# Optimization experiments

Hardware: AMD Instinct MI355X
Metric: run time of the kernel (lower is better)

Reference implementation:

```python
import jax, jax.numpy as jnp
import numpy as np

H, NB, D = 16, 64, 1024
HID = 64  # gate MLP hidden width


def setup_inputs() -> dict:
    key = jax.random.key(0)
    ks = jax.random.split(key, 10)
    B, T = 4, 2048
    delta = jax.random.normal(ks[0], (B, T, H, NB), dtype=jnp.float32)
    content_emb = jax.random.normal(ks[1], (B, T, D), dtype=jnp.float32)
    omega = jax.random.normal(ks[2], (H, NB), dtype=jnp.float32)
    # learned parameters
    log_Q = jnp.zeros((H, NB), dtype=jnp.float32)
    log_R = jnp.zeros((H, NB), dtype=jnp.float32)
    log_sigma0 = jnp.full((H, NB), -2.0, dtype=jnp.float32)
    W1 = jax.random.normal(ks[3], (D, HID), dtype=jnp.float32) / np.sqrt(D)
    b1 = jnp.zeros((HID,), dtype=jnp.float32)
    W2 = jax.random.normal(ks[4], (HID, H * NB), dtype=jnp.float32) / np.sqrt(HID)
    b2 = jnp.zeros((H * NB,), dtype=jnp.float32)
    return {"delta": delta, "content_emb": content_emb, "omega": omega,
            "log_Q": log_Q, "log_R": log_R, "log_sigma0": log_sigma0,
            "W1": W1, "b1": b1, "W2": W2, "b2": b2}


def reference(delta, content_emb, omega, log_Q, log_R, log_sigma0, W1, b1, W2, b2):
    B, T, _, _ = delta.shape
    Q = jnp.exp(log_Q)            # (H, NB)
    R = jnp.exp(log_R)            # (H, NB)
    sigma0 = jnp.exp(log_sigma0)  # (H, NB)

    theta_sq = (delta * omega) ** 2  # (B, T, H, NB)

    # landmark gate MLP (exact GELU, as torch default)
    h = jax.nn.gelu(content_emb @ W1 + b1, approximate=False)  # (B, T, HID)
    gates = jax.nn.sigmoid(h @ W2 + b2).reshape(B, T, H, NB)

    def step(sigma, xs):
        theta_sq_t, gate_t = xs  # (B, H, NB) each
        sigma = sigma + Q * theta_sq_t
        K = sigma / (sigma + R)
        sigma = sigma * (1.0 - gate_t * K)
        return sigma, sigma

    init = jnp.broadcast_to(sigma0, (B, H, NB))
    xs = (jnp.swapaxes(theta_sq, 0, 1), jnp.swapaxes(gates, 0, 1))  # (T, B, H, NB)
    _, sigma_seq = jax.lax.scan(step, init, xs)
    sigma = jnp.swapaxes(sigma_seq, 0, 1)  # (B, T, H, NB)
    return sigma, gates
```

## Files before the change

kernel.cpp:

```cpp
#include <hip/hip_runtime.h>
#include <math.h>

#define H_   16
#define NB_  64
#define D_   1024
#define HID_ 64
#define B_   4
#define T_   2048
#define ROWS (B_*T_)
#define HNB  (H_*NB_)

typedef short v8s __attribute__((ext_vector_type(8)));
typedef float v4f __attribute__((ext_vector_type(4)));

__device__ __forceinline__ float gelu_exact(float x) {
    return 0.5f * x * (1.0f + erff(x * 0.7071067811865476f));
}
__device__ __forceinline__ float sigmoidf(float x) {
    return 1.0f / (1.0f + expf(-x));
}
__device__ __forceinline__ ushort f2bf(float x) {
    union { float f; unsigned u; } v; v.f = x;
    unsigned r = v.u + 0x7fffu + ((v.u >> 16) & 1u);
    return (ushort)(r >> 16);
}

__global__ __launch_bounds__(256) void k_prep(const float* __restrict__ W1,
                                              const float* __restrict__ W2,
                                              ushort* __restrict__ w1t,
                                              ushort* __restrict__ w2t) {
    __shared__ float ls[64][65];
    const int t   = threadIdx.x;
    const int blk = blockIdx.x;
    if (blk < 16) {
        const int k0 = blk * 64;
        #pragma unroll
        for (int q = 0; q < 4; ++q) {
            int idx = q * 256 + t;
            int r = idx >> 4, c4 = idx & 15;
            *(float4*)&ls[r][c4 * 4] =
                *(const float4*)&W1[(size_t)(k0 + r) * 64 + c4 * 4];
        }
        __syncthreads();
        const int col = t >> 2, kq = t & 3;
        ushort out[16];
        #pragma unroll
        for (int e = 0; e < 16; ++e) out[e] = f2bf(ls[kq * 16 + e][col]);
        *(uint4*)&w1t[(size_t)col * 1024 + k0 + kq * 16]     = *(uint4*)&out[0];
        *(uint4*)&w1t[(size_t)col * 1024 + k0 + kq * 16 + 8] = *(uint4*)&out[8];
    } else {
        const int n0 = (blk - 16) * 64;
        #pragma unroll
        for (int q = 0; q < 4; ++q) {
            int idx = q * 256 + t;
            int r = idx >> 4, c4 = idx & 15;
            *(float4*)&ls[r][c4 * 4] =
                *(const float4*)&W2[(size_t)r * HNB + n0 + c4 * 4];
        }
        __syncthreads();
        const int n = t >> 2, kq = t & 3;
        ushort out[16];
        #pragma unroll
        for (int e = 0; e < 16; ++e) out[e] = f2bf(ls[kq * 16 + e][n]);
        *(uint4*)&w2t[(size_t)(n0 + n) * 64 + kq * 16]     = *(uint4*)&out[0];
        *(uint4*)&w2t[(size_t)(n0 + n) * 64 + kq * 16 + 8] = *(uint4*)&out[8];
    }
}

__global__ __launch_bounds__(256) void k_gemm1_mfma(const float* __restrict__ X,
                                                    const ushort* __restrict__ w1t,
                                                    const float* __restrict__ b1,
                                                    ushort* __restrict__ hbuf) {
    __shared__ ushort Al[16 * 128];
    __shared__ ushort Bl[64 * 128];
    const int t    = threadIdx.x;
    const int r0   = blockIdx.x * 16;
    const int w    = t >> 6;
    const int lane = t & 63;
    const int lo   = lane & 15;
    const int hi   = lane >> 4;
    const int arow = t >> 4, aseg = t & 15;
    const int brow = t >> 2, bseg = t & 3;

    v4f acc = {0.f,0.f,0.f,0.f};

    for (int c = 0; c < 8; ++c) {
        float xv[8];
        const float* xp = &X[(size_t)(r0 + arow) * D_ + c * 128 + aseg * 8];
        *(float4*)&xv[0] = *(const float4*)&xp[0];
        *(float4*)&xv[4] = *(const float4*)&xp[4];
        ushort wv[32];
        const ushort* wp = &w1t[(size_t)brow * 1024 + c * 128 + bseg * 32];
        #pragma unroll
        for (int i = 0; i < 4; ++i) *(uint4*)&wv[i*8] = *(const uint4*)&wp[i*8];

        __syncthreads();
        {
            const int k = aseg * 8;
            union { ushort u[8]; v8s v; } pa;
            #pragma unroll
            for (int e = 0; e < 8; ++e) pa.u[e] = f2bf(xv[e]);
            *(v8s*)&Al[arow * 128 + (k ^ ((arow & 7) << 3))] = pa.v;
        }
        #pragma unroll
        for (int j8 = 0; j8 < 4; ++j8) {
            const int k = bseg * 32 + j8 * 8;
            *(v8s*)&Bl[brow * 128 + (k ^ ((brow & 7) << 3))] = *(v8s*)&wv[j8 * 8];
        }
        __syncthreads();

        #pragma unroll
        for (int kk = 0; kk < 4; ++kk) {
            const int k  = kk * 32 + hi * 8;
            const int sw = k ^ ((lo & 7) << 3);
            v8s af = *(v8s*)&Al[lo * 128 + sw];
            v8s bf = *(v8s*)&Bl[(w * 16 + lo) * 128 + sw];
            acc = __builtin_amdgcn_mfma_f32_16x16x32_bf16(af, bf, acc, 0, 0, 0);
        }
    }
    const int col = w * 16 + lo;
    const float bb = b1[col];
    #pragma unroll
    for (int j = 0; j < 4; ++j) {
        const int row = r0 + hi * 4 + j;
        hbuf[(size_t)row * HID_ + col] = f2bf(gelu_exact(acc[j] + bb));
    }
}

__global__ __launch_bounds__(256) void k_gemm2_mfma(const ushort* __restrict__ hbuf,
                                                    const ushort* __restrict__ w2t,
                                                    const float* __restrict__ b2,
                                                    float* __restrict__ gates) {
    __shared__ ushort Ah[64 * 64];
    __shared__ ushort Bh[256 * 64];
    const int t    = threadIdx.x;
    const int r0   = (blockIdx.x >> 2) * 64;
    const int n0   = (blockIdx.x & 3) * 256;
    const int w    = t >> 6;
    const int lane = t & 63;
    const int lo   = lane & 15;
    const int hi   = lane >> 4;

    {
        const int row = t >> 2, seg = t & 3;
        uint4 v0 = *(const uint4*)&hbuf[(size_t)(r0 + row) * 64 + seg * 16];
        uint4 v1 = *(const uint4*)&hbuf[(size_t)(r0 + row) * 64 + seg * 16 + 8];
        const int sw = (row & 7) << 3;
        *(uint4*)&Ah[row * 64 + ((seg * 16) ^ sw)]     = v0;
        *(uint4*)&Ah[row * 64 + ((seg * 16 + 8) ^ sw)] = v1;
    }
    #pragma unroll
    for (int q = 0; q < 4; ++q) {
        const int pi  = q * 256 + t;
        const int n   = pi >> 2, seg = pi & 3;
        uint4 v0 = *(const uint4*)&w2t[(size_t)(n0 + n) * 64 + seg * 16];
        uint4 v1 = *(const uint4*)&w2t[(size_t)(n0 + n) * 64 + seg * 16 + 8];
        const int sw = (n & 7) << 3;
        *(uint4*)&Bh[n * 64 + ((seg * 16) ^ sw)]     = v0;
        *(uint4*)&Bh[n * 64 + ((seg * 16 + 8) ^ sw)] = v1;
    }
    __syncthreads();

    v4f acc[4][4];
    #pragma unroll
    for (int mt = 0; mt < 4; ++mt)
        #pragma unroll
        for (int nt = 0; nt < 4; ++nt) acc[mt][nt] = (v4f){0.f,0.f,0.f,0.f};

    #pragma unroll
    for (int kc = 0; kc < 2; ++kc) {
        const int k  = kc * 32 + hi * 8;
        const int sw = k ^ ((lo & 7) << 3);
        v8s af[4];
        #pragma unroll
        for (int mt = 0; mt < 4; ++mt)
            af[mt] = *(v8s*)&Ah[(mt * 16 + lo) * 64 + sw];
        #pragma unroll
        for (int nt = 0; nt < 4; ++nt) {
            v8s bf = *(v8s*)&Bh[(w * 64 + nt * 16 + lo) * 64 + sw];
            #pragma unroll
            for (int mt = 0; mt < 4; ++mt)
                acc[mt][nt] = __builtin_amdgcn_mfma_f32_16x16x32_bf16(af[mt], bf, acc[mt][nt], 0, 0, 0);
        }
    }

    #pragma unroll
    for (int nt = 0; nt < 4; ++nt) {
        const int col = n0 + w * 64 + nt * 16 + lo;
        const float bb = b2[col];
        #pragma unroll
        for (int mt = 0; mt < 4; ++mt) {
            #pragma unroll
            for (int j = 0; j < 4; ++j) {
                const int row = r0 + mt * 16 + hi * 4 + j;
                gates[(size_t)row * HNB + col] = sigmoidf(acc[mt][nt][j] + bb);
            }
        }
    }
}

#define TT_    32
#define SEGK   8
#define SEGLEN (T_/SEGK)
#define WARMT  2

#define PHASE_SYNC() { \
    asm volatile("s_waitcnt lgkmcnt(0)" ::: "memory"); \
    __builtin_amdgcn_s_barrier(); \
    asm volatile("" ::: "memory"); }

#define LD8(A, G, grp) { \
    _Pragma("unroll") \
    for (int u = 0; u < 8; ++u) { \
        A[u] = pa[((grp)*8 + u) * 128]; \
        G[u] = pa[((grp)*8 + u) * 128 + 64]; \
    } }

#define CP8(A, G, grp) { \
    _Pragma("unroll") \
    for (int u = 0; u < 8; ++u) { \
        float a   = A[u]; \
        float omg = G[u]; \
        float aR  = a + R; \
        float pc  = fmaf(omg, a, R); \
        float den = sigma + aR; \
        float s   = sigma + a; \
        float pp  = fmaf(omg, sigma, pc); \
        float rc  = __builtin_amdgcn_rcpf(den); \
        float tt  = s * pp; \
        sigma     = tt * rc; \
        ps[((grp)*8 + u) * 64] = sigma; \
    } }

#define DLOAD(tile) { \
    const int t0_ = tstart + (tile) * TT_; \
    _Pragma("unroll") \
    for (int it = 0; it < 8; ++it) \
        dreg[it] = *(const float4*)&dp[(size_t)(t0_ + it * 4 + rg) * HNB]; }

__global__ __launch_bounds__(256) void k_scan_seg4(
        const float* __restrict__ delta,
        const float* __restrict__ gates,
        const float* __restrict__ omega,
        const float* __restrict__ log_Q,
        const float* __restrict__ log_R,
        const float* __restrict__ log_s0,
        float* __restrict__ sig) {
    __shared__ float tg_lds[2][TT_][2][64];
    __shared__ float sg_lds[2][TT_][64];
    const int tid = threadIdx.x;
    const int blk = blockIdx.x;
    const int bh  = blk >> 3;
    const int seg = blk & 7;
    const int b   = bh >> 4;
    const int h   = bh & 15;
    const size_t base = (size_t)b * T_ * HNB + h * NB_;
    const int wv   = tid >> 6;
    const int lane = tid & 63;

    const int warm   = (seg == 0) ? 0 : WARMT;
    const int ntiles = SEGLEN / TT_ + warm;
    const int tstart = seg * SEGLEN - warm * TT_;

    float R = 0.f, sigma = 0.f;
    float sc0=0,sc1=0,sc2=0,sc3=0;
    const int col4 = lane & 15;
    const int rg   = lane >> 4;
    const float* dp = 0;
    float4 dreg[8];

    if (wv == 0) {
        const int hn = h * NB_ + lane;
        R     = expf(log_R[hn]);
        sigma = expf(log_s0[hn]);
    } else if (wv == 1) {
        const int hn4 = h * NB_ + col4 * 4;
        float4 om4 = *(const float4*)&omega[hn4];
        float4 lq4 = *(const float4*)&log_Q[hn4];
        sc0 = expf(lq4.x) * om4.x * om4.x;
        sc1 = expf(lq4.y) * om4.y * om4.y;
        sc2 = expf(lq4.z) * om4.z * om4.z;
        sc3 = expf(lq4.w) * om4.w * om4.w;
        dp = delta + base + col4 * 4;
        DLOAD(0);
    } else if (wv == 2) {
        dp = gates + base + col4 * 4;
        DLOAD(0);
    }

    for (int p = 0; p <= ntiles + 1; ++p) {
        if (wv == 0) {
            if (p >= 1 && p <= ntiles) {
                const int buf = (p - 1) & 1;
                const float* pa = &tg_lds[buf][0][0][lane];
                float*       ps = &sg_lds[buf][0][lane];
                float a0[8], g0[8], a1[8], g1[8];
                LD8(a0, g0, 0);
                LD8(a1, g1, 1);
                CP8(a0, g0, 0); LD8(a0, g0, 2);
                CP8(a1, g1, 1); LD8(a1, g1, 3);
                CP8(a0, g0, 2);
                CP8(a1, g1, 3);
            }
        } else if (wv == 1) {
            if (p < ntiles) {
                const int buf = p & 1;
                #pragma unroll
                for (int it = 0; it < 8; ++it) {
                    const int row = it * 4 + rg;
                    float4 d = dreg[it];
                    float4 a;
                    a.x = (sc0 * d.x) * d.x;
                    a.y = (sc1 * d.y) * d.y;
                    a.z = (sc2 * d.z) * d.z;
                    a.w = (sc3 * d.w) * d.w;
                    *(float4*)&tg_lds[buf][row][0][col4 * 4] = a;
                }
                if (p + 1 < ntiles) DLOAD(p + 1);
            }
        } else if (wv == 2) {
            if (p < ntiles) {
                const int buf = p & 1;
                #pragma unroll
                for (int it = 0; it < 8; ++it) {
                    const int row = it * 4 + rg;
                    float4 g = dreg[it];
                    float4 o;
                    o.x = 1.0f - g.x; o.y = 1.0f - g.y;
                    o.z = 1.0f - g.z; o.w = 1.0f - g.w;
                    *(float4*)&tg_lds[buf][row][1][col4 * 4] = o;
                }
                if (p + 1 < ntiles) DLOAD(p + 1);
            }
        } else {
            const int tile = p - 2;
            if (tile >= warm && tile < ntiles) {
                const int buf = p & 1;
                const int t0  = tstart + tile * TT_;
                float* op = sig + base + col4 * 4;
                #pragma unroll
                for (int it = 0; it < 8; ++it) {
                    const int row = it * 4 + rg;
                    float4 v = *(const float4*)&sg_lds[buf][row][col4 * 4];
                    *(float4*)&op[(size_t)(t0 + row) * HNB] = v;
                }
            }
        }
        PHASE_SYNC();
    }
}

extern "C" void kernel_launch(void* const* d_in, const int* in_sizes, int n_in,
                              void* d_out, int out_size, void* d_ws, size_t ws_size,
                              hipStream_t stream) {
    const float* delta   = (const float*)d_in[0];
    const float* content = (const float*)d_in[1];
    const float* omega   = (const float*)d_in[2];
    const float* log_Q   = (const float*)d_in[3];
    const float* log_R   = (const float*)d_in[4];
    const float* log_s0  = (const float*)d_in[5];
    const float* W1      = (const float*)d_in[6];
    const float* b1      = (const float*)d_in[7];
    const float* W2      = (const float*)d_in[8];
    const float* b2      = (const float*)d_in[9];

    float* sig_out   = (float*)d_out;
    float* gates_out = sig_out + (size_t)ROWS * HNB;

    const size_t n_h   = (size_t)ROWS * HID_;
    const size_t n_w1t = (size_t)HID_ * D_;
    const size_t n_w2t = (size_t)HNB * HID_;
    const size_t need  = (n_h + n_w1t + n_w2t) * sizeof(ushort);

    ushort *hbuf, *w1t, *w2t;
    if (ws_size >= need) {
        hbuf = (ushort*)d_ws;
    } else {
        hbuf = (ushort*)sig_out;
    }
    w1t = hbuf + n_h;
    w2t = w1t + n_w1t;

    k_prep<<<32, 256, 0, stream>>>(W1, W2, w1t, w2t);
    k_gemm1_mfma<<<ROWS / 16, 256, 0, stream>>>(content, w1t, b1, hbuf);
    k_gemm2_mfma<<<(ROWS / 64) * 4, 256, 0, stream>>>(hbuf, w2t, b2, gates_out);
    k_scan_seg4<<<B_ * H_ * SEGK, 256, 0, stream>>>(delta, gates_out, omega,
                                                    log_Q, log_R, log_s0, sig_out);
}
```

Measured before the change: 55.34 us.

## Feed scan a bf16 copy of gates and remap scan block order

The gate GEMM now also writes a bf16 copy of the sigmoid gates to workspace, and a new scan kernel reads that half-width copy instead of the fp32 gates, unpacking it in a dedicated wave. The block index mapping is also permuted so that consecutive blocks cover different (b,h) pairs. The aim is to cut scan-side memory traffic, at the cost of an extra 16 MB write in the GEMM and reduced gate precision inside the recurrence. The new path only runs when the workspace is large enough; otherwise the old path is used.

```diff
diff --git a/kernel.cpp b/kernel.cpp
--- a/kernel.cpp
+++ b/kernel.cpp
@@ -130,7 +130,8 @@
 __global__ __launch_bounds__(256) void k_gemm2_mfma(const ushort* __restrict__ hbuf,
                                                     const ushort* __restrict__ w2t,
                                                     const float* __restrict__ b2,
-                                                    float* __restrict__ gates) {
+                                                    float* __restrict__ gates,
+                                                    ushort* __restrict__ gbf) {
     __shared__ ushort Ah[64 * 64];
     __shared__ ushort Bh[256 * 64];
     const int t    = threadIdx.x;
@@ -193,7 +194,9 @@
             #pragma unroll
             for (int j = 0; j < 4; ++j) {
                 const int row = r0 + mt * 16 + hi * 4 + j;
-                gates[(size_t)row * HNB + col] = sigmoidf(acc[mt][nt][j] + bb);
+                float gv = sigmoidf(acc[mt][nt][j] + bb);
+                gates[(size_t)row * HNB + col] = gv;
+                if (gbf) gbf[(size_t)row * HNB + col] = f2bf(gv);
             }
         }
     }
@@ -237,6 +240,133 @@
     _Pragma("unroll") \
     for (int it = 0; it < 8; ++it) \
         dreg[it] = *(const float4*)&dp[(size_t)(t0_ + it * 4 + rg) * HNB]; }
+
+#define GLOAD(tile) { \
+    const int t0_ = tstart + (tile) * TT_; \
+    _Pragma("unroll") \
+    for (int it = 0; it < 4; ++it) \
+        greg[it] = *(const uint4*)&gp2[(size_t)(t0_ + it * 8 + rg8) * HNB]; }
+
+__global__ __launch_bounds__(256) void k_scan_seg6(
+        const float* __restrict__ delta,
+        const ushort* __restrict__ gbf,
+        const float* __restrict__ omega,
+        const float* __restrict__ log_Q,
+        const float* __restrict__ log_R,
+        const float* __restrict__ log_s0,
+        float* __restrict__ sig) {
+    __shared__ float tg_lds[2][TT_][2][64];
+    __shared__ float sg_lds[2][TT_][64];
+    const int tid = threadIdx.x;
+    const int blk = blockIdx.x;
+    const int bh  = (blk & 7) * 8 + (blk >> 6);
+    const int seg = (blk >> 3) & 7;
+    const int b   = bh >> 4;
+    const int h   = bh & 15;
+    const size_t base = (size_t)b * T_ * HNB + h * NB_;
+    const int wv   = tid >> 6;
+    const int lane = tid & 63;
+
+    const int warm   = (seg == 0) ? 0 : WARMT;
+    const int ntiles = SEGLEN / TT_ + warm;
+    const int tstart = seg * SEGLEN - warm * TT_;
+
+    float R = 0.f, sigma = 0.f;
+    float sc0=0,sc1=0,sc2=0,sc3=0;
+    const int col4 = lane & 15;
+    const int rg   = lane >> 4;
+    const int col8 = lane & 7;
+    const int rg8  = lane >> 3;
+    const float* dp = 0;
+    const ushort* gp2 = 0;
+    float4 dreg[8];
+    uint4  greg[4];
+
+    if (wv == 0) {
+        const int hn = h * NB_ + lane;
+        R     = expf(log_R[hn]);
+        sigma = expf(log_s0[hn]);
+    } else if (wv == 1) {
+        const int hn4 = h * NB_ + col4 * 4;
+        float4 om4 = *(const float4*)&omega[hn4];
+        float4 lq4 = *(const float4*)&log_Q[hn4];
+        sc0 = expf(lq4.x) * om4.x * om4.x;
+        sc1 = expf(lq4.y) * om4.y * om4.y;
+        sc2 = expf(lq4.z) * om4.z * om4.z;
+        sc3 = expf(lq4.w) * om4.w * om4.w;
+        dp = delta + base + col4 * 4;
+        DLOAD(0);
+    } else if (wv == 2) {
+        gp2 = gbf + base + col8 * 8;
+        GLOAD(0);
+    }
+
+    for (int p = 0; p <= ntiles + 1; ++p) {
+        if (wv == 0) {
+            if (p >= 1 && p <= ntiles) {
+                const int buf = (p - 1) & 1;
+                const float* pa = &tg_lds[buf][0][0][lane];
+                float*       ps = &sg_lds[buf][0][lane];
+                float a0[8], g0[8], a1[8], g1[8];
+                LD8(a0, g0, 0);
+                LD8(a1, g1, 1);
+                CP8(a0, g0, 0); LD8(a0, g0, 2);
+                CP8(a1, g1, 1); LD8(a1, g1, 3);
+                CP8(a0, g0, 2);
+                CP8(a1, g1, 3);
+            }
+        } else if (wv == 1) {
+            if (p < ntiles) {
+                const int buf = p & 1;
+                #pragma unroll
+                for (int it = 0; it < 8; ++it) {
+                    const int row = it * 4 + rg;
+                    float4 d = dreg[it];
+                    float4 a;
+                    a.x = (sc0 * d.x) * d.x;
+                    a.y = (sc1 * d.y) * d.y;
+                    a.z = (sc2 * d.z) * d.z;
+                    a.w = (sc3 * d.w) * d.w;
+                    *(float4*)&tg_lds[buf][row][0][col4 * 4] = a;
+                }
+                if (p + 1 < ntiles) DLOAD(p + 1);
+            }
+        } else if (wv == 2) {
+            if (p < ntiles) {
+                const int buf = p & 1;
+                #pragma unroll
+                for (int it = 0; it < 4; ++it) {
+                    const int row = it * 8 + rg8;
+                    unsigned uu[4] = {greg[it].x, greg[it].y, greg[it].z, greg[it].w};
+                    float o[8];
+                    #pragma unroll
+                    for (int j = 0; j < 4; ++j) {
+                        union { unsigned u; float f; } c;
+                        c.u = uu[j] << 16;          o[2*j]   = 1.0f - c.f;
+                        c.u = uu[j] & 0xffff0000u;  o[2*j+1] = 1.0f - c.f;
+                    }
+                    *(float4*)&tg_lds[buf][row][1][col8 * 8]     = *(float4*)&o[0];
+                    *(float4*)&tg_lds[buf][row][1][col8 * 8 + 4] = *(float4*)&o[4];
+                }
+                if (p + 1 < ntiles) GLOAD(p + 1);
+            }
+        } else {
+            const int tile = p - 2;
+            if (tile >= warm && tile < ntiles) {
+                const int buf = p & 1;
+                const int t0  = tstart + tile * TT_;
+                float* op = sig + base + col4 * 4;
+                #pragma unroll
+                for (int it = 0; it < 8; ++it) {
+                    const int row = it * 4 + rg;
+                    float4 v = *(const float4*)&sg_lds[buf][row][col4 * 4];
+                    *(float4*)&op[(size_t)(t0 + row) * HNB] = v;
+                }
+            }
+        }
+        PHASE_SYNC();
+    }
+}
 
 __global__ __launch_bounds__(256) void k_scan_seg4(
         const float* __restrict__ delta,
@@ -370,20 +500,32 @@
     const size_t n_h   = (size_t)ROWS * HID_;
     const size_t n_w1t = (size_t)HID_ * D_;
     const size_t n_w2t = (size_t)HNB * HID_;
-    const size_t need  = (n_h + n_w1t + n_w2t) * sizeof(ushort);
-
-    ushort *hbuf, *w1t, *w2t;
-    if (ws_size >= need) {
-        hbuf = (ushort*)d_ws;
+    const size_t n_gbf = (size_t)ROWS * HNB;
+    const size_t need_full = (n_h + n_w1t + n_w2t + n_gbf) * sizeof(ushort);
+    const size_t need_min  = (n_h + n_w1t + n_w2t) * sizeof(ushort);
+
+    if (ws_size >= need_full) {
+        ushort* hbuf = (ushort*)d_ws;
+        ushort* w1t  = hbuf + n_h;
+        ushort* w2t  = w1t + n_w1t;
+        ushort* gbf  = w2t + n_w2t;
+        k_prep<<<32, 256, 0, stream>>>(W1, W2, w1t, w2t);
+        k_gemm1_mfma<<<ROWS / 16, 256, 0, stream>>>(content, w1t, b1, hbuf);
+        k_gemm2_mfma<<<(ROWS / 64) * 4, 256, 0, stream>>>(hbuf, w2t, b2,
+                                                          gates_out, gbf);
+        k_scan_seg6<<<B_ * H_ * SEGK, 256, 0, stream>>>(delta, gbf, omega,
+                                                        log_Q, log_R, log_s0,
+                                                        sig_out);
     } else {
-        hbuf = (ushort*)sig_out;
-    }
-    w1t = hbuf + n_h;
-    w2t = w1t + n_w1t;
-
-    k_prep<<<32, 256, 0, stream>>>(W1, W2, w1t, w2t);
-    k_gemm1_mfma<<<ROWS / 16, 256, 0, stream>>>(content, w1t, b1, hbuf);
-    k_gemm2_mfma<<<(ROWS / 64) * 4, 256, 0, stream>>>(hbuf, w2t, b2, gates_out);
-    k_scan_seg4<<<B_ * H_ * SEGK, 256, 0, stream>>>(delta, gates_out, omega,
-                                                    log_Q, log_R, log_s0, sig_out);
-}
+        ushort* hbuf = (ws_size >= need_min) ? (ushort*)d_ws : (ushort*)sig_out;
+        ushort* w1t  = hbuf + n_h;
+        ushort* w2t  = w1t + n_w1t;
+        k_prep<<<32, 256, 0, stream>>>(W1, W2, w1t, w2t);
+        k_gemm1_mfma<<<ROWS / 16, 256, 0, stream>>>(content, w1t, b1, hbuf);
+        k_gemm2_mfma<<<(ROWS / 64) * 4, 256, 0, stream>>>(hbuf, w2t, b2,
+                                                          gates_out, nullptr);
+        k_scan_seg4<<<B_ * H_ * SEGK, 256, 0, stream>>>(delta, gates_out, omega,
+                                                        log_Q, log_R, log_s0,
+                                                        sig_out);
+    }
+}
```

After: 55.45 us. Within noise of the previous version (+0.2%).
